# Performance work log

Measured on AMD Instinct MI355X. Metric: run time of the kernel, lower is better.

The kernel has to match this reference:

```python
import jax, jax.numpy as jnp
import numpy as np
from jax import lax

BETA_CONTENT = 1.0   # content_addressing default beta
BETA_TOPK = 10.0     # top_k_attention default beta
GAMMA = 1.5          # location sharpening
ERASE = 0.5          # erase_strength for write
EPS = 1e-8
NEG = -1.0e9

N_SLOTS, SLOT_D, BATCH, K = 65536, 256, 512, 64


def _l2norm(x):
    # F.normalize: x / max(||x||, 1e-12)
    n = jnp.sqrt(jnp.sum(x * x, axis=-1, keepdims=True))
    return x / jnp.maximum(n, 1e-12)


def setup_inputs() -> dict:
    key = jax.random.key(0)
    k1, k2, k3, k4, k5 = jax.random.split(key, 5)
    return {
        "memory": jax.random.normal(k1, (N_SLOTS, SLOT_D), dtype=jnp.float32) * 0.1,
        "query": jax.random.normal(k2, (BATCH, SLOT_D), dtype=jnp.float32),
        "value": jax.random.normal(k3, (BATCH, SLOT_D), dtype=jnp.float32),
        "prev_weights": jax.random.uniform(k4, (BATCH, N_SLOTS), dtype=jnp.float32),
        "shift_weights": jax.random.uniform(k5, (3,), dtype=jnp.float32),
        "k": K,
    }


def reference(memory, query, value, prev_weights, shift_weights, k):
    B, N = query.shape[0], memory.shape[0]
    # --- content addressing: cosine sim + softmax ---
    qn = _l2norm(query)                      # [B,D]
    mn = _l2norm(memory)                     # [N,D]
    sim = qn @ mn.T                          # [B,N]
    w_content = jax.nn.softmax(BETA_CONTENT * sim, axis=-1)
    read_content = w_content @ memory        # [B,D] read via content weights

    # --- top-k attention: soft threshold mask + softmax ---
    kk = min(int(k), N)
    topk_vals, _ = lax.top_k(sim, kk)        # [B,kk]
    thr = topk_vals[:, -1:]                  # kth largest similarity
    mask = jax.nn.sigmoid(BETA_TOPK * (sim - thr))
    w_topk = jax.nn.softmax(BETA_TOPK * sim + (1.0 - mask) * NEG, axis=-1)
    read_topk = w_topk @ memory              # [B,D]

    # --- location addressing: conv1d shift (padding=1) + gamma sharpen ---
    p = jnp.pad(prev_weights, ((0, 0), (1, 1)))  # [B,N+2]
    shifted = (p[:, :-2] * shift_weights[0]
               + p[:, 1:-1] * shift_weights[1]
               + p[:, 2:] * shift_weights[2])     # [B,N]
    sharp = shifted ** GAMMA
    w_loc = sharp / (jnp.sum(sharp, axis=-1, keepdims=True) + EPS)

    # --- write: softmax(address), multiplicative erase, additive write ---
    w_write = jax.nn.softmax(w_loc, axis=-1)          # write() softmaxes its input
    erase_factor = jnp.prod(1.0 - w_write * ERASE, axis=0)   # [N] sequential erases fused
    new_mem = memory * erase_factor[:, None] + w_write.T @ value  # [N,D]

    return jnp.concatenate([read_content.reshape(-1),
                            read_topk.reshape(-1),
                            new_mem.reshape(-1)])
```

## Files before the change

### kernel.cpp

```cpp
#include <hip/hip_runtime.h>
#include <math.h>

#define BATCH   512
#define NSLOTS  65536
#define DIM     256

#define RB      64
#define NROWG   (BATCH/RB)
#define NCG     64
#define CPG     (NSLOTS/NCG)
#define ST      32
#define NTILES  (CPG/ST)
#define DELTA   0.009f

#define WS_QN   0
#define WS_RN   (WS_QN + BATCH*DIM)
#define WS_WST  (WS_RN + NSLOTS)
#define WS_DEN  (WS_WST + BATCH*4)
#define WS_SST  (WS_DEN + BATCH)
#define WS_VT   (WS_SST + BATCH*NCG*16*4)
#define WS_MN   (WS_VT + (BATCH*DIM)/2)
#define WS_MT   (WS_MN + ((size_t)NSLOTS*DIM)/2)

typedef __attribute__((ext_vector_type(8))) short bf16x8;
typedef __attribute__((ext_vector_type(4))) float f32x4;

__device__ inline unsigned short f2b(float x){
  unsigned u = __float_as_uint(x);
  unsigned r = u + 0x7FFFu + ((u >> 16) & 1u);
  return (unsigned short)(r >> 16);
}
__device__ inline float b2f(unsigned short b){
  return __uint_as_float(((unsigned)b) << 16);
}

__device__ __forceinline__ void gl16(const void* g, void* l){
  __builtin_amdgcn_global_load_lds(
      (__attribute__((address_space(1))) void*)g,
      (__attribute__((address_space(3))) void*)l, 16, 0, 0);
}

#define SBAR_LGKM() do{ asm volatile("s_waitcnt lgkmcnt(0)" ::: "memory"); \
                        __builtin_amdgcn_s_barrier();                      \
                        asm volatile("" ::: "memory"); }while(0)
#define SBAR_ALL()  do{ asm volatile("s_waitcnt vmcnt(0) lgkmcnt(0)" ::: "memory"); \
                        __builtin_amdgcn_s_barrier();                               \
                        asm volatile("" ::: "memory"); }while(0)

__global__ __launch_bounds__(256) void k_qnorm(const float* __restrict__ q, float* __restrict__ qn){
  int b = blockIdx.x, t = threadIdx.x;
  float v = q[b*DIM + t];
  __shared__ float red[256];
  red[t] = v*v;
  __syncthreads();
  for (int s = 128; s > 0; s >>= 1){
    if (t < s) red[t] += red[t+s];
    __syncthreads();
  }
  float n = fmaxf(sqrtf(red[0]), 1e-12f);
  qn[b*DIM + t] = v / n;
}

__global__ __launch_bounds__(256) void k_mnprep(const float* __restrict__ mem,
                                                float* __restrict__ rn,
                                                unsigned short* __restrict__ MN){
  __shared__ float rns[64];
  int t = threadIdx.x;
  int s0 = blockIdx.x * 64;
  int w = t >> 6, ln = t & 63;
  #pragma unroll
  for (int it = 0; it < 16; ++it){
    int r = it*4 + w;
    float4 v = ((const float4*)(mem + (size_t)(s0 + r)*DIM))[ln];
    float s = v.x*v.x + v.y*v.y + v.z*v.z + v.w*v.w;
    #pragma unroll
    for (int off = 32; off > 0; off >>= 1) s += __shfl_xor(s, off, 64);
    if (ln == 0){
      float inv = 1.0f / fmaxf(sqrtf(s), 1e-12f);
      rns[r] = inv; rn[s0 + r] = inv;
    }
  }
  __syncthreads();
  #pragma unroll
  for (int j = 0; j < 8; ++j){
    int id = j*256 + t;
    int r = id >> 5;
    int c = id & 31;
    float inv = rns[r];
    const float4* p = (const float4*)(mem + (size_t)(s0 + r)*DIM + c*8);
    float4 a = p[0], b = p[1];
    bf16x8 o;
    o[0]=(short)f2b(a.x*inv); o[1]=(short)f2b(a.y*inv); o[2]=(short)f2b(a.z*inv); o[3]=(short)f2b(a.w*inv);
    o[4]=(short)f2b(b.x*inv); o[5]=(short)f2b(b.y*inv); o[6]=(short)f2b(b.z*inv); o[7]=(short)f2b(b.w*inv);
    *(bf16x8*)&MN[(size_t)(s0 + r)*DIM + ((c ^ (r & 7))*8)] = o;
  }
}

__global__ __launch_bounds__(256) void k_mtprep(const float* __restrict__ mem, unsigned short* __restrict__ MT){
  __shared__ __align__(16) unsigned short tile[64][68];
  int sb = (blockIdx.x >> 2)*64, dd = (blockIdx.x & 3)*64;
  int t = threadIdx.x;
  int w = t >> 6, ln = t & 63;
  #pragma unroll
  for (int k = 0; k < 4; ++k){
    int sl = w*16 + k*4 + (ln >> 4);
    int doff = (ln & 15)*4;
    float4 f = *(const float4*)&mem[(size_t)(sb + sl)*DIM + dd + doff];
    tile[doff+0][sl] = f2b(f.x);
    tile[doff+1][sl] = f2b(f.y);
    tile[doff+2][sl] = f2b(f.z);
    tile[doff+3][sl] = f2b(f.w);
  }
  __syncthreads();
  #pragma unroll
  for (int k = 0; k < 4; ++k){
    int dl = w*16 + k*4 + (ln >> 4);
    int boff = (ln & 15)*4;
    int B = boff >> 5;
    int p = (boff >> 3) & 3;
    int pp = p ^ ((dl >> 1) & 3);
    int off = B*32 + pp*8 + (boff & 7);
    *(short4*)&MT[(size_t)(dd + dl)*NSLOTS + sb + off] = *(const short4*)&tile[dl][boff];
  }
}

__global__ __launch_bounds__(256) void k_prep(const float* __restrict__ val, unsigned short* __restrict__ VT){
  __shared__ __align__(16) unsigned short tile[64][68];
  int bb = (blockIdx.x >> 2)*64, dd = (blockIdx.x & 3)*64;
  int t = threadIdx.x;
  int w = t >> 6, ln = t & 63;
  #pragma unroll
  for (int k = 0; k < 4; ++k){
    int bl = w*16 + k*4 + (ln >> 4);
    int doff = (ln & 15)*4;
    float4 f = *(const float4*)&val[(size_t)(bb + bl)*DIM + dd + doff];
    tile[doff+0][bl] = f2b(f.x);
    tile[doff+1][bl] = f2b(f.y);
    tile[doff+2][bl] = f2b(f.z);
    tile[doff+3][bl] = f2b(f.w);
  }
  __syncthreads();
  #pragma unroll
  for (int k = 0; k < 4; ++k){
    int dl = w*16 + k*4 + (ln >> 4);
    int boff = (ln & 15)*4;
    *(short4*)&VT[(size_t)(dd + dl)*BATCH + bb + boff] = *(const short4*)&tile[dl][boff];
  }
}

__global__ __launch_bounds__(256) void k_wstats(const float* __restrict__ prev, const float* __restrict__ sw,
                                                float* __restrict__ wst){
  int b = blockIdx.x, t = threadIdx.x;
  float s0 = sw[0], s1 = sw[1], s2 = sw[2];
  const float* p = prev + (size_t)b*NSLOTS;
  const float4* p4 = (const float4*)p;
  __shared__ float rs[256];
  float lsum = 0.f;
  for (int i4 = t; i4 < NSLOTS/4; i4 += 256){
    float4 f = p4[i4];
    float lft = (i4 > 0) ? p[4*i4 - 1] : 0.f;
    float rgt = (i4 < NSLOTS/4 - 1) ? p[4*i4 + 4] : 0.f;
    float sh0 = s0*lft + s1*f.x + s2*f.y;
    float sh1 = s0*f.x + s1*f.y + s2*f.z;
    float sh2 = s0*f.y + s1*f.z + s2*f.w;
    float sh3 = s0*f.z + s1*f.w + s2*rgt;
    lsum += sh0*sqrtf(sh0) + sh1*sqrtf(sh1) + sh2*sqrtf(sh2) + sh3*sqrtf(sh3);
  }
  rs[t] = lsum;
  __syncthreads();
  for (int s = 128; s > 0; s >>= 1){
    if (t < s) rs[t] += rs[t+s];
    __syncthreads();
  }
  float inv_d = 1.0f / (rs[0] + 1e-8f);
  __syncthreads();
  float lz = 0.f;
  for (int i4 = t; i4 < NSLOTS/4; i4 += 256){
    float4 f = p4[i4];
    float lft = (i4 > 0) ? p[4*i4 - 1] : 0.f;
    float rgt = (i4 < NSLOTS/4 - 1) ? p[4*i4 + 4] : 0.f;
    float sh0 = s0*lft + s1*f.x + s2*f.y;
    float sh1 = s0*f.x + s1*f.y + s2*f.z;
    float sh2 = s0*f.y + s1*f.z + s2*f.w;
    float sh3 = s0*f.z + s1*f.w + s2*rgt;
    lz += __expf(sh0*sqrtf(sh0)*inv_d) + __expf(sh1*sqrtf(sh1)*inv_d)
        + __expf(sh2*sqrtf(sh2)*inv_d) + __expf(sh3*sqrtf(sh3)*inv_d);
  }
  rs[t] = lz;
  __syncthreads();
  for (int s = 128; s > 0; s >>= 1){
    if (t < s) rs[t] += rs[t+s];
    __syncthreads();
  }
  if (t == 0){
    float4 o; o.x = inv_d; o.y = 1.0f/rs[0]; o.z = 0.f; o.w = 0.f;
    ((float4*)wst)[b] = o;
  }
}

__global__ __launch_bounds__(256, 2) void k_simfused(
    const float* __restrict__ qn,
    const unsigned short* __restrict__ MN,
    const unsigned short* __restrict__ MT,
    float* __restrict__ outc, float* __restrict__ denom, float* __restrict__ sst)
{
  __shared__ __align__(16) unsigned short Ms[2][32*256];
  __shared__ __align__(16) unsigned short Md[2][256*32];
  __shared__ __align__(16) unsigned short Plds[64*40];

  int cg = blockIdx.x, rg = blockIdx.y;
  int t = threadIdx.x;
  int w = t >> 6;
  int lane = t & 63;
  int l = lane & 15;
  int q = lane >> 4;
  int row0 = rg * RB;

  bf16x8 qa[8];
  {
    int qrow = row0 + 16*w + l;
    #pragma unroll
    for (int kk = 0; kk < 8; ++kk){
      const float4* qp = (const float4*)&qn[(size_t)qrow*DIM + 32*kk + 8*q];
      float4 a0 = qp[0], a1 = qp[1];
      bf16x8 v;
      v[0]=(short)f2b(a0.x); v[1]=(short)f2b(a0.y); v[2]=(short)f2b(a0.z); v[3]=(short)f2b(a0.w);
      v[4]=(short)f2b(a1.x); v[5]=(short)f2b(a1.y); v[6]=(short)f2b(a1.z); v[7]=(short)f2b(a1.w);
      qa[kk] = v;
    }
  }

  const char* msP = (const char*)MN + (size_t)cg*CPG*512 + (size_t)w*4096 + (size_t)lane*16;
  const char* mtP = (const char*)MT + (size_t)(w*64 + (lane>>2))*((size_t)NSLOTS*2)
                                    + (size_t)cg*CPG*2 + (size_t)(lane&3)*16;

  auto STAGE = [&](int tl, int buf){
    size_t mso = (size_t)tl*16384;
    size_t mto = (size_t)tl*64;
    #pragma unroll
    for (int j = 0; j < 4; ++j)
      gl16(msP + mso + (size_t)j*1024, &Ms[buf][w*2048 + j*512]);
    #pragma unroll
    for (int j = 0; j < 4; ++j)
      gl16(mtP + mto + (size_t)j*2097152, &Md[buf][w*2048 + j*512]);
  };

  f32x4 accO[16];
  #pragma unroll
  for (int c = 0; c < 16; ++c) accO[c] = (f32x4){0.f,0.f,0.f,0.f};

  float dsum[4] = {0.f,0.f,0.f,0.f};
  float tv0[4] = {-1e30f,-1e30f,-1e30f,-1e30f}, tv1[4] = {-1e30f,-1e30f,-1e30f,-1e30f};
  int   ti0[4] = {0,0,0,0}, ti1[4] = {0,0,0,0};

  STAGE(0, 0);
  SBAR_ALL();

  int r7 = l & 7;
  int sw2 = (q ^ ((l >> 1) & 3)) * 8;

  for (int tile = 0; tile < NTILES; ++tile){
    int cur = tile & 1;
    if (tile + 1 < NTILES) STAGE(tile + 1, cur ^ 1);
    int i0 = cg*CPG + tile*ST;

    const unsigned short* msb = &Ms[cur][0];
    f32x4 S0 = (f32x4){0.f,0.f,0.f,0.f}, S1 = (f32x4){0.f,0.f,0.f,0.f};
    #pragma unroll
    for (int kk = 0; kk < 8; ++kk){
      int c0 = ((4*kk + q) ^ r7) * 8;
      bf16x8 b0 = *(const bf16x8*)&msb[(l     )*256 + c0];
      bf16x8 b1 = *(const bf16x8*)&msb[(16 + l)*256 + c0];
      S0 = __builtin_amdgcn_mfma_f32_16x16x32_bf16(qa[kk], b0, S0, 0, 0, 0);
      S1 = __builtin_amdgcn_mfma_f32_16x16x32_bf16(qa[kk], b1, S1, 0, 0, 0);
    }

    #pragma unroll
    for (int c = 0; c < 2; ++c){
      int slot = i0 + 16*c + l;
      #pragma unroll
      for (int reg = 0; reg < 4; ++reg){
        float v = (c == 0) ? S0[reg] : S1[reg];
        bool g0 = v > tv0[reg];
        bool g1 = v > tv1[reg];
        float ov0 = tv0[reg]; int oi0 = ti0[reg];
        tv1[reg] = g0 ? ov0 : (g1 ? v : tv1[reg]);
        ti1[reg] = g0 ? oi0 : (g1 ? slot : ti1[reg]);
        tv0[reg] = g0 ? v : tv0[reg];
        ti0[reg] = g0 ? slot : ti0[reg];
        unsigned short wb = f2b(__expf(v));
        dsum[reg] += b2f(wb);
        Plds[(16*w + 4*q + reg)*40 + 16*c + l] = (short)wb;
      }
    }
    SBAR_LGKM();

    bf16x8 pa = *(const bf16x8*)&Plds[(16*w + l)*40 + 8*q];
    const unsigned short* mdb = &Md[cur][0];
    #pragma unroll
    for (int ct = 0; ct < 16; ++ct){
      bf16x8 b = *(const bf16x8*)&mdb[(16*ct + l)*32 + sw2];
      accO[ct] = __builtin_amdgcn_mfma_f32_16x16x32_bf16(pa, b, accO[ct], 0, 0, 0);
    }
    SBAR_ALL();
  }

  #pragma unroll
  for (int reg = 0; reg < 4; ++reg){
    float s = dsum[reg];
    s += __shfl_xor(s, 1, 64); s += __shfl_xor(s, 2, 64);
    s += __shfl_xor(s, 4, 64); s += __shfl_xor(s, 8, 64);
    if (l == 0) atomicAdd(&denom[row0 + 16*w + 4*q + reg], s);
  }
  #pragma unroll
  for (int reg = 0; reg < 4; ++reg){
    int row = row0 + 16*w + 4*q + reg;
    size_t base = (((size_t)row*NCG + cg)*16 + l)*2;
    float2* S2 = (float2*)sst;
    S2[base + 0] = make_float2(tv0[reg], __int_as_float(ti0[reg]));
    S2[base + 1] = make_float2(tv1[reg], __int_as_float(ti1[reg]));
  }
  #pragma unroll
  for (int ct = 0; ct < 16; ++ct){
    #pragma unroll
    for (int reg = 0; reg < 4; ++reg){
      int row = row0 + 16*w + 4*q + reg;
      atomicAdd(&outc[(size_t)row*DIM + 16*ct + l], accO[ct][reg]);
    }
  }
}

__global__ __launch_bounds__(256) void k_finish(const float* __restrict__ sst, const float* __restrict__ denom,
                                                const float* __restrict__ qn, const float* __restrict__ rn,
                                                const float* __restrict__ mem,
                                                float* __restrict__ outc, float* __restrict__ outk){
  int row = blockIdx.x, t = threadIdx.x;
  __shared__ float red[256];
  __shared__ int cnt;
  __shared__ int cidx[128];
  __shared__ float csim[128];
  __shared__ int bestIdx;
  const float2* S = (const float2*)sst + (size_t)row*NCG*16*2;
  float2 e[8];
  float lmax = -1e30f;
  #pragma unroll
  for (int k = 0; k < 8; ++k){ e[k] = S[t*8 + k]; lmax = fmaxf(lmax, e[k].x); }
  red[t] = lmax;
  __syncthreads();
  for (int s = 128; s > 0; s >>= 1){
    if (t < s) red[t] = fmaxf(red[t], red[t+s]);
    __syncthreads();
  }
  float M = red[0];
  if (t == 0) cnt = 0;
  __syncthreads();
  #pragma unroll
  for (int k = 0; k < 8; ++k){
    if (e[k].x >= M - DELTA){
      int p = atomicAdd(&cnt, 1);
      if (p < 128) cidx[p] = __float_as_int(e[k].y);
    }
  }
  __syncthreads();
  int n = min(cnt, 128);
  int wv = t >> 6, ln = t & 63;
  for (int ci = wv; ci < n; ci += 4){
    int slot = cidx[ci];
    float4 a = ((const float4*)&qn[(size_t)row*DIM])[ln];
    float4 b = ((const float4*)&mem[(size_t)slot*DIM])[ln];
    float s = a.x*b.x + a.y*b.y + a.z*b.z + a.w*b.w;
    #pragma unroll
    for (int off = 32; off > 0; off >>= 1) s += __shfl_xor(s, off, 64);
    if (ln == 0) csim[ci] = s * rn[slot];
  }
  __syncthreads();
  if (t == 0){
    float bv = -1e30f; int bi = 0x7fffffff;
    for (int i = 0; i < n; ++i){
      float v = csim[i]; int id = cidx[i];
      if (v > bv || (v == bv && id < bi)){ bv = v; bi = id; }
    }
    bestIdx = bi;
  }
  __syncthreads();
  float inv = 1.0f / denom[row];
  outc[(size_t)row*DIM + t] *= inv;
  outk[(size_t)row*DIM + t] = mem[(size_t)bestIdx*DIM + t];
}

__global__ __launch_bounds__(256) void k_newmem(const float* __restrict__ mem,
                                                const unsigned short* __restrict__ VT,
                                                const float* __restrict__ prev, const float* __restrict__ sw,
                                                const float* __restrict__ wst, float* __restrict__ outm){
  __shared__ __align__(16) short WA[64*40];
  __shared__ float ep[4][64];
  __shared__ float eprodS[64];

  int t = threadIdx.x;
  int i0 = blockIdx.x * 64;
  int sl = t & 63;
  int bg = t >> 6;
  int i  = i0 + sl;
  int w = t >> 6;
  int lane = t & 63;
  int l = lane & 15, q = lane >> 4;
  float s0 = sw[0], s1 = sw[1], s2 = sw[2];

  f32x4 accO[16];
  #pragma unroll
  for (int c = 0; c < 16; ++c) accO[c] = (f32x4){0.f,0.f,0.f,0.f};
  float epl = 1.0f;

  for (int c = 0; c < 16; ++c){
    __syncthreads();
    bf16x8 wv;
    #pragma unroll
    for (int j = 0; j < 8; ++j){
      int b = c*32 + bg*8 + j;
      const float* p = prev + (size_t)b*NSLOTS;
      float a  = (i > 0) ? p[i-1] : 0.f;
      float ce = p[i];
      float d  = (i < NSLOTS-1) ? p[i+1] : 0.f;
      float sh = s0*a + s1*ce + s2*d;
      float sharp = sh*sqrtf(sh);
      float4 st = ((const float4*)wst)[b];
      float wf = __expf(sharp*st.x)*st.y;
      epl *= (1.0f - 0.5f*wf);
      wv[j] = (short)f2b(wf);
    }
    *(bf16x8*)&WA[sl*40 + bg*8] = wv;
    __syncthreads();
    bf16x8 af = *(const bf16x8*)&WA[(16*w + l)*40 + 8*q];
    #pragma unroll
    for (int ct = 0; ct < 16; ++ct){
      bf16x8 bfg = *(const bf16x8*)&VT[(size_t)(16*ct + l)*BATCH + c*32 + 8*q];
      accO[ct] = __builtin_amdgcn_mfma_f32_16x16x32_bf16(af, bfg, accO[ct], 0, 0, 0);
    }
  }
  ep[bg][sl] = epl;
  __syncthreads();
  if (t < 64) eprodS[t] = ep[0][t]*ep[1][t]*ep[2][t]*ep[3][t];
  __syncthreads();

  #pragma unroll
  for (int reg = 0; reg < 4; ++reg){
    int slot = i0 + 16*w + 4*q + reg;
    float e = eprodS[16*w + 4*q + reg];
    #pragma unroll
    for (int ct = 0; ct < 16; ++ct){
      int d = 16*ct + l;
      outm[(size_t)slot*DIM + d] = mem[(size_t)slot*DIM + d]*e + accO[ct][reg];
    }
  }
}

extern "C" void kernel_launch(void* const* d_in, const int* in_sizes, int n_in,
                              void* d_out, int out_size, void* d_ws, size_t ws_size,
                              hipStream_t stream){
  const float* mem  = (const float*)d_in[0];
  const float* qry  = (const float*)d_in[1];
  const float* val  = (const float*)d_in[2];
  const float* prev = (const float*)d_in[3];
  const float* sw   = (const float*)d_in[4];
  float* out = (float*)d_out;
  float* ws  = (float*)d_ws;

  float* qn   = ws + WS_QN;
  float* rn   = ws + WS_RN;
  float* wst  = ws + WS_WST;
  float* den  = ws + WS_DEN;
  float* sst  = ws + WS_SST;
  unsigned short* VT = (unsigned short*)(ws + WS_VT);
  unsigned short* MN = (unsigned short*)(ws + WS_MN);
  unsigned short* MT = (unsigned short*)(ws + WS_MT);

  float* out_content = out;
  float* out_topk    = out + BATCH*DIM;
  float* out_newmem  = out + 2*BATCH*DIM;

  hipMemsetAsync(out_content, 0, BATCH*DIM*sizeof(float), stream);
  hipMemsetAsync(den, 0, BATCH*sizeof(float), stream);
  hipLaunchKernelGGL(k_qnorm,   dim3(BATCH),       dim3(DIM), 0, stream, qry, qn);
  hipLaunchKernelGGL(k_mnprep,  dim3(NSLOTS/64),   dim3(256), 0, stream, mem, rn, MN);
  hipLaunchKernelGGL(k_mtprep,  dim3((NSLOTS/64)*4), dim3(256), 0, stream, mem, MT);
  hipLaunchKernelGGL(k_prep,    dim3(32),          dim3(256), 0, stream, val, VT);
  hipLaunchKernelGGL(k_wstats,  dim3(BATCH),       dim3(256), 0, stream, prev, sw, wst);
  hipLaunchKernelGGL(k_simfused,dim3(NCG, NROWG),  dim3(256), 0, stream, qn, MN, MT, out_content, den, sst);
  hipLaunchKernelGGL(k_finish,  dim3(BATCH),       dim3(256), 0, stream, sst, den, qn, rn, mem, out_content, out_topk);
  hipLaunchKernelGGL(k_newmem,  dim3(NSLOTS/64),   dim3(256), 0, stream, mem, VT, prev, sw, wst, out_newmem);
}
```

Before: 616.3 us.

## Compute MFMA A-fragments directly in registers, drop LDS staging and barriers in k_newmem

Each lane now computes the write weights for exactly the slot and batch elements its MFMA A-fragment needs. This removes the shared-memory transpose buffer and the two __syncthreads per iteration, and the erase-factor product is reduced with wave shuffles instead of LDS. A launch-bounds occupancy hint of 4 blocks per SM is also added. The trade-off is that global loads of prev become less coalesced: a wave's 16 consecutive slots are spread across 4 batch rows, so each row is read in 64-byte chunks instead of 256-byte ones.

```diff
diff --git a/kernel.cpp b/kernel.cpp
--- a/kernel.cpp
+++ b/kernel.cpp
@@ -388,22 +388,16 @@
   outk[(size_t)row*DIM + t] = mem[(size_t)bestIdx*DIM + t];
 }
 
-__global__ __launch_bounds__(256) void k_newmem(const float* __restrict__ mem,
+__global__ __launch_bounds__(256, 4) void k_newmem(const float* __restrict__ mem,
                                                 const unsigned short* __restrict__ VT,
                                                 const float* __restrict__ prev, const float* __restrict__ sw,
                                                 const float* __restrict__ wst, float* __restrict__ outm){
-  __shared__ __align__(16) short WA[64*40];
-  __shared__ float ep[4][64];
-  __shared__ float eprodS[64];
-
   int t = threadIdx.x;
   int i0 = blockIdx.x * 64;
-  int sl = t & 63;
-  int bg = t >> 6;
-  int i  = i0 + sl;
   int w = t >> 6;
   int lane = t & 63;
   int l = lane & 15, q = lane >> 4;
+  int slot = i0 + 16*w + l;
   float s0 = sw[0], s1 = sw[1], s2 = sw[2];
 
   f32x4 accO[16];
@@ -411,45 +405,43 @@
   for (int c = 0; c < 16; ++c) accO[c] = (f32x4){0.f,0.f,0.f,0.f};
   float epl = 1.0f;
 
+  const float* pc = prev + (size_t)slot;
+
+  #pragma unroll 1
   for (int c = 0; c < 16; ++c){
-    __syncthreads();
-    bf16x8 wv;
+    bf16x8 af;
     #pragma unroll
     for (int j = 0; j < 8; ++j){
-      int b = c*32 + bg*8 + j;
-      const float* p = prev + (size_t)b*NSLOTS;
-      float a  = (i > 0) ? p[i-1] : 0.f;
-      float ce = p[i];
-      float d  = (i < NSLOTS-1) ? p[i+1] : 0.f;
+      int b = c*32 + q*8 + j;
+      const float* p = pc + (size_t)b*NSLOTS;
+      float a  = (slot > 0) ? p[-1] : 0.f;
+      float ce = p[0];
+      float d  = (slot < NSLOTS-1) ? p[1] : 0.f;
       float sh = s0*a + s1*ce + s2*d;
       float sharp = sh*sqrtf(sh);
-      float4 st = ((const float4*)wst)[b];
+      float2 st = *(const float2*)&wst[b*4];
       float wf = __expf(sharp*st.x)*st.y;
       epl *= (1.0f - 0.5f*wf);
-      wv[j] = (short)f2b(wf);
-    }
-    *(bf16x8*)&WA[sl*40 + bg*8] = wv;
-    __syncthreads();
-    bf16x8 af = *(const bf16x8*)&WA[(16*w + l)*40 + 8*q];
+      af[j] = (short)f2b(wf);
+    }
     #pragma unroll
     for (int ct = 0; ct < 16; ++ct){
       bf16x8 bfg = *(const bf16x8*)&VT[(size_t)(16*ct + l)*BATCH + c*32 + 8*q];
       accO[ct] = __builtin_amdgcn_mfma_f32_16x16x32_bf16(af, bfg, accO[ct], 0, 0, 0);
     }
   }
-  ep[bg][sl] = epl;
-  __syncthreads();
-  if (t < 64) eprodS[t] = ep[0][t]*ep[1][t]*ep[2][t]*ep[3][t];
-  __syncthreads();
+
+  epl *= __shfl_xor(epl, 16, 64);
+  epl *= __shfl_xor(epl, 32, 64);
 
   #pragma unroll
   for (int reg = 0; reg < 4; ++reg){
-    int slot = i0 + 16*w + 4*q + reg;
-    float e = eprodS[16*w + 4*q + reg];
+    int so = i0 + 16*w + 4*q + reg;
+    float e = __shfl(epl, 4*q + reg, 64);
     #pragma unroll
     for (int ct = 0; ct < 16; ++ct){
       int d = 16*ct + l;
-      outm[(size_t)slot*DIM + d] = mem[(size_t)slot*DIM + d]*e + accO[ct][reg];
+      outm[(size_t)so*DIM + d] = mem[(size_t)so*DIM + d]*e + accO[ct][reg];
     }
   }
 }
```

After: 611.9 us. No clear change (-0.7%).
